# Kernel optimization log

Measured on AMD Instinct MI355X. Metric: run time of the kernel, lower is better.

Reference implementation:

```python
import jax, jax.numpy as jnp
import numpy as np


def _gumbel(key, shape):
    # -log(Exp(1)) == standard Gumbel; matches torch's -empty.exponential_().log()
    u = jax.random.uniform(key, shape, minval=1e-10, maxval=1.0)
    return -jnp.log(-jnp.log(u))


def setup_inputs() -> dict:
    key = jax.random.key(0)
    dims = [(1026, 1024), (3074, 1024), (5122, 512)]
    names = ['wc1', 'wc2', 'wd1', 'wd2', 'gc1', 'gc2', 'gd1', 'gd2']
    inp = {}
    k = key
    for li, (din, dout) in enumerate(dims, start=1):
        for nm in names:
            k, sub = jax.random.split(k)
            if nm.startswith('w'):
                inp[f'l{li}_{nm}'] = jax.random.normal(sub, (din, dout), dtype=jnp.float32)
            else:
                inp[f'l{li}_{nm}'] = _gumbel(sub, (din, dout)).astype(jnp.float32)
    k, kx, kw = jax.random.split(k, 3)
    inp['x'] = jax.random.uniform(kx, (32768, 512), dtype=jnp.float32)
    inp['lin_w'] = jax.random.uniform(kw, (1, 1024), dtype=jnp.float32)
    inp['tau'] = 1
    return inp


def _st_gate(w, g, tau):
    # hard gumbel-softmax over axis 0 with straight-through estimator
    y = jax.nn.softmax((w + g) / tau, axis=0)
    hard = jax.nn.one_hot(jnp.argmax(y, axis=0), w.shape[0], dtype=y.dtype).T
    return hard + y - jax.lax.stop_gradient(y)


def _logic_layer(h, ws, gs, tau, skip):
    wc1, wc2, wd1, wd2 = ws
    gc1, gc2, gd1, gd2 = gs
    c = (h @ _st_gate(wc1, gc1, tau)) * (h @ _st_gate(wc2, gc2, tau))  # AND
    a = h @ _st_gate(wd1, gd1, tau)
    b = h @ _st_gate(wd2, gd2, tau)
    d = 1.0 - (1.0 - a) * (1.0 - b)  # OR
    parts = [h, c, d] if skip else [c, d]
    return jnp.concatenate(parts, axis=-1)


def reference(x, l1_wc1, l1_wc2, l1_wd1, l1_wd2, l1_gc1, l1_gc2, l1_gd1, l1_gd2,
              l2_wc1, l2_wc2, l2_wd1, l2_wd2, l2_gc1, l2_gc2, l2_gd1, l2_gd2,
              l3_wc1, l3_wc2, l3_wd1, l3_wd2, l3_gc1, l3_gc2, l3_gd1, l3_gd2,
              lin_w, tau):
    t = jnp.asarray(tau, dtype=x.dtype)
    B = x.shape[0]
    # InputAugmentor: [x, 1-x, 1, 0]
    h = jnp.concatenate([x, 1.0 - x, jnp.ones((B, 1), x.dtype), jnp.zeros((B, 1), x.dtype)], axis=-1)
    layers = [
        ((l1_wc1, l1_wc2, l1_wd1, l1_wd2), (l1_gc1, l1_gc2, l1_gd1, l1_gd2), True),
        ((l2_wc1, l2_wc2, l2_wd1, l2_wd2), (l2_gc1, l2_gc2, l2_gd1, l2_gd2), True),
        ((l3_wc1, l3_wc2, l3_wd1, l3_wd2), (l3_gc1, l3_gc2, l3_gd1, l3_gd2), False),
    ]
    for ws, gs, skip in layers:
        h = _logic_layer(h, ws, gs, t, skip)
    # nonnegative == False -> weight used as-is
    return (h @ lin_w.T).squeeze(-1)
```

## Files before the change

kernel.cpp:

```cpp
#include <hip/hip_runtime.h>
#include <hip/hip_fp16.h>
#include <stdint.h>


struct GatePtrs {
    const float* w[12];
    const float* g[12];
};

__device__ __forceinline__ unsigned int sortkey(float f) {
    unsigned int u = __float_as_uint(f);
    return u ^ ((u & 0x80000000u) ? 0xFFFFFFFFu : 0x80000000u);
}

__global__ __launch_bounds__(256, 2) void argmax_part(GatePtrs gp,
                                                      unsigned long long* __restrict__ part) {
    const int dins[3]  = {1026, 3074, 5122};
    const int chs[3]   = {65, 193, 321};
    const int pbs[3]   = {0, 266240, 1056768};
    int bid = blockIdx.x;
    int layer, slot, chunk, c4, dout;
    if (bid < 260) {
        layer = 0; slot = bid / 65; chunk = bid - slot * 65;
        c4 = threadIdx.x; dout = 1024;
    } else if (bid < 1032) {
        layer = 1; int r = bid - 260; slot = r / 193; chunk = r - slot * 193;
        c4 = threadIdx.x; dout = 1024;
    } else {
        layer = 2; int r = bid - 1032; slot = r / 161; int cb = r - slot * 161;
        int sub = threadIdx.x >> 7; c4 = threadIdx.x & 127; dout = 512;
        chunk = cb * 2 + sub;
        if (chunk >= 321) return;
    }
    int gate = layer * 4 + slot;
    int din = dins[layer], ch = chs[layer];
    int s4 = dout >> 2;
    int r0 = chunk * 16;
    int n  = min(16, din - r0);
    const float4* __restrict__ wp = (const float4*)gp.w[gate] + (size_t)r0 * s4 + c4;
    const float4* __restrict__ gq = (const float4*)gp.g[gate] + (size_t)r0 * s4 + c4;
    float bx = -3.4e38f, by = bx, bz = bx, bw = bx;
    int ix = r0, iy = r0, iz = r0, iw = r0;
    if (n == 16) {
        float4 wv[16], gv[16];
        const size_t rs = (size_t)s4;
        #pragma unroll
        for (int k = 0; k < 16; ++k) {
            wv[k] = wp[(size_t)k * rs];
            gv[k] = gq[(size_t)k * rs];
        }
        asm volatile("" ::: "memory");
        #pragma unroll
        for (int k = 0; k < 16; ++k) {
            int i = r0 + k;
            float vx = wv[k].x + gv[k].x;
            float vy = wv[k].y + gv[k].y;
            float vz = wv[k].z + gv[k].z;
            float vw = wv[k].w + gv[k].w;
            if (vx > bx) { bx = vx; ix = i; }
            if (vy > by) { by = vy; iy = i; }
            if (vz > bz) { bz = vz; iz = i; }
            if (vw > bw) { bw = vw; iw = i; }
        }
    } else {
        for (int m = 0; m < n; ++m) {
            float4 wv = wp[(size_t)m * s4];
            float4 gv = gq[(size_t)m * s4];
            int i = r0 + m;
            float vx = wv.x + gv.x, vy = wv.y + gv.y;
            float vz = wv.z + gv.z, vw = wv.w + gv.w;
            if (vx > bx) { bx = vx; ix = i; }
            if (vy > by) { by = vy; iy = i; }
            if (vz > bz) { bz = vz; iz = i; }
            if (vw > bw) { bw = vw; iw = i; }
        }
    }
    unsigned long long* dst = part + pbs[layer]
                            + ((size_t)(slot * ch + chunk)) * dout + 4 * c4;
    dst[0] = ((unsigned long long)sortkey(bx) << 32) | (unsigned int)ix;
    dst[1] = ((unsigned long long)sortkey(by) << 32) | (unsigned int)iy;
    dst[2] = ((unsigned long long)sortkey(bz) << 32) | (unsigned int)iz;
    dst[3] = ((unsigned long long)sortkey(bw) << 32) | (unsigned int)iw;
}

__global__ __launch_bounds__(256) void reduce_pairs2(const unsigned long long* __restrict__ part,
                                                     unsigned short* __restrict__ pf) {
    __shared__ unsigned long long red[256];
    int t = threadIdx.x;
    int k = t >> 5, gi = t & 31;
    int C = blockIdx.x * 32;
    int l, s, g0, half, dout, ch, pb;
    if (C < 4096)      { l = 0; s = C >> 10;          g0 = C & 1023;          half = 1024; dout = 1024; ch = 65;  pb = 0; }
    else if (C < 8192) { l = 1; s = (C - 4096) >> 10; g0 = (C - 4096) & 1023; half = 1024; dout = 1024; ch = 193; pb = 266240; }
    else               { l = 2; s = (C - 8192) >> 9;  g0 = (C - 8192) & 511;  half = 512;  dout = 512;  ch = 321; pb = 1056768; }
    int g = g0 + gi;
    const unsigned long long* __restrict__ p = part + pb + (size_t)(s * ch) * dout + g;
    unsigned long long best = 0;
    for (int c = k; c < ch; c += 8) {
        unsigned long long v = p[(size_t)c * dout];
        if ((unsigned int)(v >> 32) > (unsigned int)(best >> 32)) best = v;
    }
    red[t] = best;
    __syncthreads();
    #pragma unroll
    for (int st = 4; st >= 1; st >>= 1) {
        if (k < st) {
            unsigned long long o = red[t + st * 32];
            if ((unsigned int)(o >> 32) > (unsigned int)(best >> 32)) best = o;
            red[t] = best;
        }
        __syncthreads();
    }
    if (k == 0) {
        int type = s >> 1, e = s & 1;
        int j = 2 * (l * 2048 + type * half + g) + e;
        pf[j] = (unsigned short)best;
    }
}

__global__ __launch_bounds__(256) void argmax_atomic(GatePtrs gp,
                                                     unsigned long long* __restrict__ packed) {
    const int dins[3]  = {1026, 3074, 5122};
    const int douts[3] = {1024, 1024, 512};
    const int offs[3]  = {0, 4096, 8192};
    int gate = blockIdx.z, layer = gate >> 2;
    int din = dins[layer], dout = douts[layer];
    int c2 = blockIdx.x * 256 + threadIdx.x;
    int r0 = blockIdx.y * 64;
    if (2 * c2 >= dout || r0 >= din) return;
    int r1 = min(r0 + 64, din);
    const float* __restrict__ w = gp.w[gate];
    const float* __restrict__ g = gp.g[gate];
    float bx = -3.4e38f, by = -3.4e38f;
    int rx = r0, ry = r0;
    #pragma unroll 8
    for (int i = r0; i < r1; ++i) {
        float2 wv = *(const float2*)(w + (size_t)i * dout + 2 * c2);
        float2 gv = *(const float2*)(g + (size_t)i * dout + 2 * c2);
        float vx = wv.x + gv.x, vy = wv.y + gv.y;
        if (vx > bx) { bx = vx; rx = i; }
        if (vy > by) { by = vy; ry = i; }
    }
    unsigned long long* dst = packed + offs[layer] + (gate & 3) * dout + 2 * c2;
    atomicMax(dst, ((unsigned long long)sortkey(bx) << 32)
                   | (unsigned long long)(0xFFFFFFFFu - (unsigned int)rx));
    atomicMax(dst + 1, ((unsigned long long)sortkey(by) << 32)
                   | (unsigned long long)(0xFFFFFFFFu - (unsigned int)ry));
}

__global__ __launch_bounds__(256) void convert_fb(const unsigned long long* __restrict__ packed,
                                                  ushort2* __restrict__ pf) {
    int i = blockIdx.x * 256 + threadIdx.x;
    if (i >= 5120) return;
    int l    = (i < 2048) ? 0 : ((i < 4096) ? 1 : 2);
    int half = (l == 2) ? 512 : 1024;
    int r    = i - l * 2048;
    int type = (r >= half) ? 1 : 0;
    int g    = r - type * half;
    int o1   = l * 4096 + 2 * type * half + g;
    int o2   = o1 + half;
    unsigned int i1 = 0xFFFFFFFFu - (unsigned int)(packed[o1] & 0xFFFFFFFFull);
    unsigned int i2 = 0xFFFFFFFFu - (unsigned int)(packed[o2] & 0xFFFFFFFFull);
    pf[i] = make_ushort2((unsigned short)i1, (unsigned short)i2);
}

__device__ __forceinline__ __half2 bc(unsigned int u) { return __builtin_bit_cast(__half2, u); }
__device__ __forceinline__ unsigned int cb(__half2 h) { return __builtin_bit_cast(unsigned int, h); }

__device__ __forceinline__ uint2 gat(const char* hb, unsigned int s) {
    return *(const uint2*)(hb + (s << 3));
}
__device__ __forceinline__ uint2 andg(uint2 a, uint2 b) {
    return make_uint2(cb(__hmul2(bc(a.x), bc(b.x))), cb(__hmul2(bc(a.y), bc(b.y))));
}
__device__ __forceinline__ uint2 org(uint2 a, uint2 b) {
    __half2 one = __float2half2_rn(1.0f);
    __half2 lo = __hsub2(one, __hmul2(__hsub2(one, bc(a.x)), __hsub2(one, bc(b.x))));
    __half2 hi = __hsub2(one, __hmul2(__hsub2(one, bc(a.y)), __hsub2(one, bc(b.y))));
    return make_uint2(cb(lo), cb(hi));
}

__global__ __launch_bounds__(512) void forward_kernel(const float* __restrict__ x,
                                                      const float* __restrict__ lin_w,
                                                      const ushort2* __restrict__ pairs,
                                                      float* __restrict__ out) {
    __shared__ uint2 h[5122];
    __shared__ float4 red[8];
    const int t  = threadIdx.x;
    const int r0 = blockIdx.x * 4;
    const char* hb = (const char*)h;

    float xa = x[(size_t)(r0 + 0) * 512 + t];
    float xb = x[(size_t)(r0 + 1) * 512 + t];
    float xc = x[(size_t)(r0 + 2) * 512 + t];
    float xd = x[(size_t)(r0 + 3) * 512 + t];
    ushort2 pa0 = pairs[t], pa1 = pairs[512 + t];
    ushort2 po0 = pairs[1024 + t], po1 = pairs[1536 + t];
    h[t]       = make_uint2(cb(__floats2half2_rn(xa, xb)), cb(__floats2half2_rn(xc, xd)));
    h[512 + t] = make_uint2(cb(__floats2half2_rn(1.f - xa, 1.f - xb)),
                            cb(__floats2half2_rn(1.f - xc, 1.f - xd)));
    if (t == 0) {
        unsigned int o = cb(__float2half2_rn(1.0f));
        h[1024] = make_uint2(o, o);
        h[1025] = make_uint2(0u, 0u);
    }
    __syncthreads();

    {
        uint2 a0 = andg(gat(hb, pa0.x), gat(hb, pa0.y));
        uint2 a1 = andg(gat(hb, pa1.x), gat(hb, pa1.y));
        uint2 o0 = org(gat(hb, po0.x), gat(hb, po0.y));
        uint2 o1 = org(gat(hb, po1.x), gat(hb, po1.y));
        h[1026 + t] = a0; h[1538 + t] = a1;
        h[2050 + t] = o0; h[2562 + t] = o1;
    }
    ushort2 qa0 = pairs[2048 + t], qa1 = pairs[2560 + t];
    ushort2 qo0 = pairs[3072 + t], qo1 = pairs[3584 + t];
    __syncthreads();

    {
        uint2 a0 = andg(gat(hb, qa0.x), gat(hb, qa0.y));
        uint2 a1 = andg(gat(hb, qa1.x), gat(hb, qa1.y));
        uint2 o0 = org(gat(hb, qo0.x), gat(hb, qo0.y));
        uint2 o1 = org(gat(hb, qo1.x), gat(hb, qo1.y));
        h[3074 + t] = a0; h[3586 + t] = a1;
        h[4098 + t] = o0; h[4610 + t] = o1;
    }
    ushort2 za = pairs[4096 + t], zo = pairs[4608 + t];
    float wA = lin_w[t], wO = lin_w[512 + t];
    __syncthreads();

    uint2 cg = andg(gat(hb, za.x), gat(hb, za.y));
    uint2 dg = org(gat(hb, zo.x), gat(hb, zo.y));
    float2 cl = __half22float2(bc(cg.x)), ch2 = __half22float2(bc(cg.y));
    float2 dl = __half22float2(bc(dg.x)), dh = __half22float2(bc(dg.y));
    float4 s;
    s.x = wA * cl.x  + wO * dl.x;
    s.y = wA * cl.y  + wO * dl.y;
    s.z = wA * ch2.x + wO * dh.x;
    s.w = wA * ch2.y + wO * dh.y;

    #pragma unroll
    for (int off = 32; off > 0; off >>= 1) {
        s.x += __shfl_down(s.x, off, 64);
        s.y += __shfl_down(s.y, off, 64);
        s.z += __shfl_down(s.z, off, 64);
        s.w += __shfl_down(s.w, off, 64);
    }
    if ((t & 63) == 0) red[t >> 6] = s;
    __syncthreads();
    if (t == 0) {
        float4 tot = red[0];
        #pragma unroll
        for (int i = 1; i < 8; ++i) {
            tot.x += red[i].x; tot.y += red[i].y;
            tot.z += red[i].z; tot.w += red[i].w;
        }
        *(float4*)(out + r0) = tot;
    }
}

extern "C" void kernel_launch(void* const* d_in, const int* in_sizes, int n_in,
                              void* d_out, int out_size, void* d_ws, size_t ws_size,
                              hipStream_t stream) {
    GatePtrs gp;
    for (int l = 0; l < 3; ++l)
        for (int s = 0; s < 4; ++s) {
            gp.w[l * 4 + s] = (const float*)d_in[l * 8 + s];
            gp.g[l * 4 + s] = (const float*)d_in[l * 8 + 4 + s];
        }
    const float* x     = (const float*)d_in[24];
    const float* lin_w = (const float*)d_in[25];
    float* out = (float*)d_out;

    const size_t partBytes = 1714176ull * 8ull;
    if (ws_size >= partBytes + 20480) {
        unsigned long long* part = (unsigned long long*)d_ws;
        unsigned short* pf = (unsigned short*)((char*)d_ws + partBytes);
        argmax_part<<<1676, 256, 0, stream>>>(gp, part);
        reduce_pairs2<<<320, 256, 0, stream>>>(part, pf);
        forward_kernel<<<8192, 512, 0, stream>>>(x, lin_w, (const ushort2*)pf, out);
    } else {
        unsigned long long* packed = (unsigned long long*)d_ws;
        ushort2* pf = (ushort2*)((char*)d_ws + 10240 * 8);
        hipMemsetAsync(d_ws, 0, 10240 * 8, stream);
        dim3 ga(2, 81, 12);
        argmax_atomic<<<ga, 256, 0, stream>>>(gp, packed);
        convert_fb<<<20, 256, 0, stream>>>(packed, pf);
        forward_kernel<<<8192, 512, 0, stream>>>(x, lin_w, (const ushort2*)pf, out);
    }
}
```

Baseline: 343.5 us.

## Software-pipeline argmax loads with inline asm ring buffer and manual vmcnt waits

Replaces the load-all-then-compute loop in the argmax partial kernel with an 8-deep ring of inline-asm global loads and explicit s_waitcnt vmcnt stages, so compute on early rows overlaps later loads. This halves the register buffer and drops the occupancy hint from launch_bounds. It aims to cut VGPR pressure and raise occupancy while keeping many loads in flight. It relies on hand-counted vmcnt values, and the inline asm stops the compiler from scheduling or checking these loads.

```diff
diff --git a/kernel.cpp b/kernel.cpp
--- a/kernel.cpp
+++ b/kernel.cpp
@@ -8,13 +8,15 @@
     const float* g[12];
 };
 
+typedef float f32x4 __attribute__((ext_vector_type(4)));
+
 __device__ __forceinline__ unsigned int sortkey(float f) {
     unsigned int u = __float_as_uint(f);
     return u ^ ((u & 0x80000000u) ? 0xFFFFFFFFu : 0x80000000u);
 }
 
-__global__ __launch_bounds__(256, 2) void argmax_part(GatePtrs gp,
-                                                      unsigned long long* __restrict__ part) {
+__global__ __launch_bounds__(256) void argmax_part(GatePtrs gp,
+                                                   unsigned long long* __restrict__ part) {
     const int dins[3]  = {1026, 3074, 5122};
     const int chs[3]   = {65, 193, 321};
     const int pbs[3]   = {0, 266240, 1056768};
@@ -42,26 +44,48 @@
     float bx = -3.4e38f, by = bx, bz = bx, bw = bx;
     int ix = r0, iy = r0, iz = r0, iw = r0;
     if (n == 16) {
-        float4 wv[16], gv[16];
+        f32x4 wv[8], gv[8];
         const size_t rs = (size_t)s4;
-        #pragma unroll
-        for (int k = 0; k < 16; ++k) {
-            wv[k] = wp[(size_t)k * rs];
-            gv[k] = gq[(size_t)k * rs];
-        }
-        asm volatile("" ::: "memory");
-        #pragma unroll
-        for (int k = 0; k < 16; ++k) {
-            int i = r0 + k;
-            float vx = wv[k].x + gv[k].x;
-            float vy = wv[k].y + gv[k].y;
-            float vz = wv[k].z + gv[k].z;
-            float vw = wv[k].w + gv[k].w;
-            if (vx > bx) { bx = vx; ix = i; }
-            if (vy > by) { by = vy; iy = i; }
-            if (vz > bz) { bz = vz; iz = i; }
-            if (vw > bw) { bw = vw; iw = i; }
-        }
+#define ISSUE(k)                                                               \
+        asm volatile("global_load_dwordx4 %0, %1, off"                         \
+                     : "=v"(wv[(k) & 7]) : "v"(wp + (size_t)(k) * rs));        \
+        asm volatile("global_load_dwordx4 %0, %1, off"                         \
+                     : "=v"(gv[(k) & 7]) : "v"(gq + (size_t)(k) * rs));
+#define STAGE(k, NW)                                                           \
+        asm volatile("s_waitcnt vmcnt(" #NW ")");                              \
+        __builtin_amdgcn_sched_barrier(0);                                     \
+        {                                                                      \
+            const int kk = (k);                                                \
+            int i = r0 + kk;                                                   \
+            float vx = wv[kk & 7].x + gv[kk & 7].x;                            \
+            float vy = wv[kk & 7].y + gv[kk & 7].y;                            \
+            float vz = wv[kk & 7].z + gv[kk & 7].z;                            \
+            float vw = wv[kk & 7].w + gv[kk & 7].w;                            \
+            if (vx > bx) { bx = vx; ix = i; }    \
+            if (vy > by) { by = vy; iy = i; }                                  \
+            if (vz > bz) { bz = vz; iz = i; }                                  \
+            if (vw > bw) { bw = vw; iw = i; }                                  \
+        }
+        ISSUE(0) ISSUE(1) ISSUE(2) ISSUE(3)
+        ISSUE(4) ISSUE(5) ISSUE(6) ISSUE(7)
+        STAGE(0, 14) ISSUE(8)
+        STAGE(1, 14) ISSUE(9)
+        STAGE(2, 14) ISSUE(10)
+        STAGE(3, 14) ISSUE(11)
+        STAGE(4, 14) ISSUE(12)
+        STAGE(5, 14) ISSUE(13)
+        STAGE(6, 14) ISSUE(14)
+        STAGE(7, 14) ISSUE(15)
+        STAGE(8, 14)
+        STAGE(9, 12)
+        STAGE(10, 10)
+        STAGE(11, 8)
+        STAGE(12, 6)
+        STAGE(13, 4)
+        STAGE(14, 2)
+        STAGE(15, 0)
+#undef ISSUE
+#undef STAGE
     } else {
         for (int m = 0; m < n; ++m) {
             float4 wv = wp[(size_t)m * s4];
```

Result: no change. 341.4 us (-0.6%).
